# Kernel tuning notes

Measured on AMD Instinct MI355X. Metric: run time of the kernel, lower is better.

The kernel has to match this reference:

```python
import jax, jax.numpy as jnp
import numpy as np

EPS_NORM = 1e-12  # F.normalize eps
SINK_EPS = 0.1    # entropic regularization
THRESH = 0.01
MAX_ITERS = 100


def _l2_normalize(x):
    n = jnp.linalg.norm(x, axis=1, keepdims=True)
    return x / jnp.maximum(n, EPS_NORM)


def _sinkhorn(K, u, v):
    # K: [M, N], u: [M], v: [N]. Mirrors the torch loop with early stop on err < thresh.
    def cond(state):
        i, r, c, err = state
        return jnp.logical_and(i < MAX_ITERS, err >= THRESH)

    def body(state):
        i, r, c, _ = state
        r0 = r
        r = u / (K @ c)          # [M]
        c = v / (K.T @ r)        # [N]
        err = jnp.mean(jnp.abs(r - r0))
        return (i + 1, r, c, err)

    init = (jnp.int32(0), jnp.ones_like(u), jnp.ones_like(v), jnp.float32(1e9))
    _, r, c, _ = jax.lax.while_loop(cond, body, init)
    return jnp.outer(r, c) * K   # [M, N]


def _ot(src, tgt):
    # src: [M, D] (gt cluster centers), tgt: [N, D] (local features)
    s = _l2_normalize(src)
    t = _l2_normalize(tgt)
    sim = s @ t.T                         # [M, N], differentiable
    M, N = sim.shape
    u = jnp.full((M,), 1.0 / M, sim.dtype)
    v = jnp.full((N,), 1.0 / N, sim.dtype)
    K = jax.lax.stop_gradient(jnp.exp(-(1.0 - sim) / SINK_EPS))  # no_grad in torch
    T = jax.lax.stop_gradient(_sinkhorn(K, u, v))
    return jnp.sum(T * sim)


def setup_inputs() -> dict:
    key = jax.random.key(0)
    k1, k2, k3, k4 = jax.random.split(key, 4)
    E, B, D = 3, 4096, 1024
    M, N = 5, 256
    return {
        "feature": jax.random.normal(k1, (E, B, D), jnp.float32),
        "gt": jax.random.normal(k2, (E, B, D), jnp.float32),
        "gt_local": jax.random.normal(k3, (E, M, D), jnp.float32),
        "feature_local": jax.random.normal(k4, (E, N, D), jnp.float32),
    }


def reference(feature, gt, gt_local, feature_local):
    E = feature.shape[0]
    # global term: (1/E) * sum_e mean_b sum_d feature*gt
    loss_global = jnp.mean(jnp.sum(feature * gt, axis=-1))
    # local OT term per extractor: OT(gt_local, feature_local) * 2, then / E
    ot_vals = jax.vmap(_ot)(gt_local, feature_local)  # [E]
    loss_local = jnp.sum(ot_vals * 2.0) / E
    return loss_global + loss_local * 0.1
```

## Files before the change

### kernel.cpp

```cpp
#include <hip/hip_runtime.h>
#include <math.h>

#define NSIM_BLOCKS 48
#define NDOT_BLOCKS 512
#define TOTAL_F4 3145728

__global__ __launch_bounds__(256) void fused_main(
    const float4* __restrict__ f4, const float4* __restrict__ g4,
    const float* __restrict__ gt_local, const float* __restrict__ feat_local,
    float* __restrict__ ws_partials, float* __restrict__ ws_sim)
{
    __shared__ float s_sh[5 * 1024];
    __shared__ float rns_sh[5];
    __shared__ float red_sh[4];
    const int tid = threadIdx.x;
    const int lane = tid & 63;
    const int wid = tid >> 6;

    if (blockIdx.x < NSIM_BLOCKS) {
        const int b = blockIdx.x;
        const int e = b >> 4;
        const int chunk = b & 15;
        const float* sbase = gt_local + e * 5 * 1024;
        for (int idx = tid; idx < 5120; idx += 256) s_sh[idx] = sbase[idx];
        __syncthreads();
        for (int m = wid; m < 5; m += 4) {
            float acc = 0.f;
            #pragma unroll
            for (int k = 0; k < 16; ++k) {
                float v = s_sh[m * 1024 + lane + 64 * k];
                acc += v * v;
            }
            #pragma unroll
            for (int o = 32; o; o >>= 1) acc += __shfl_xor(acc, o);
            if (lane == 0) rns_sh[m] = 1.f / fmaxf(sqrtf(acc), 1e-12f);
        }
        __syncthreads();
        for (int rr = 0; rr < 4; ++rr) {
            const int n = chunk * 16 + wid * 4 + rr;
            const float* trow = feat_local + (e * 256 + n) * 1024;
            float a0 = 0.f, a1 = 0.f, a2 = 0.f, a3 = 0.f, a4 = 0.f, at = 0.f;
            #pragma unroll
            for (int k = 0; k < 16; ++k) {
                const int d = lane + 64 * k;
                const float tv = trow[d];
                at += tv * tv;
                a0 += tv * s_sh[d];
                a1 += tv * s_sh[1024 + d];
                a2 += tv * s_sh[2048 + d];
                a3 += tv * s_sh[3072 + d];
                a4 += tv * s_sh[4096 + d];
            }
            #pragma unroll
            for (int o = 32; o; o >>= 1) {
                at += __shfl_xor(at, o);
                a0 += __shfl_xor(a0, o);
                a1 += __shfl_xor(a1, o);
                a2 += __shfl_xor(a2, o);
                a3 += __shfl_xor(a3, o);
                a4 += __shfl_xor(a4, o);
            }
            if (lane == 0) {
                const float rnt = 1.f / fmaxf(sqrtf(at), 1e-12f);
                float* dst = ws_sim + e * 5 * 256 + n;
                dst[0]    = a0 * rns_sh[0] * rnt;
                dst[256]  = a1 * rns_sh[1] * rnt;
                dst[512]  = a2 * rns_sh[2] * rnt;
                dst[768]  = a3 * rns_sh[3] * rnt;
                dst[1024] = a4 * rns_sh[4] * rnt;
            }
        }
    } else {
        const int d = blockIdx.x - NSIM_BLOCKS;
        float acc = 0.f;
        const int stride = NDOT_BLOCKS * 256;
        for (int i = d * 256 + tid; i < TOTAL_F4; i += stride) {
            const float4 a = f4[i];
            const float4 b = g4[i];
            acc += a.x * b.x + a.y * b.y + a.z * b.z + a.w * b.w;
        }
        #pragma unroll
        for (int o = 32; o; o >>= 1) acc += __shfl_xor(acc, o);
        if (lane == 0) red_sh[wid] = acc;
        __syncthreads();
        if (tid == 0)
            ws_partials[d] = red_sh[0] + red_sh[1] + red_sh[2] + red_sh[3];
    }
}

__global__ __launch_bounds__(256) void finalize_kernel(
    const float* __restrict__ ws_partials, const float* __restrict__ ws_sim,
    float* __restrict__ out)
{
    __shared__ float ot_sh[3];
    __shared__ double g_sh;
    const int tid = threadIdx.x;
    const int lane = tid & 63;
    const int wid = tid >> 6;

    if (wid < 3) {
        const int e = wid;
        float K[5][4], S[5][4];
        #pragma unroll
        for (int m = 0; m < 5; ++m)
            #pragma unroll
            for (int j = 0; j < 4; ++j) {
                const float s = ws_sim[(e * 5 + m) * 256 + lane + 64 * j];
                S[m][j] = s;
                K[m][j] = expf(-(1.0f - s) / 0.1f);
            }
        float r[5] = {1.f, 1.f, 1.f, 1.f, 1.f};
        float c[4] = {1.f, 1.f, 1.f, 1.f};
        float err;
        int it = 0;
        do {
            float r0[5];
            #pragma unroll
            for (int m = 0; m < 5; ++m) r0[m] = r[m];
            #pragma unroll
            for (int m = 0; m < 5; ++m) {
                float p = K[m][0] * c[0] + K[m][1] * c[1] +
                          K[m][2] * c[2] + K[m][3] * c[3];
                #pragma unroll
                for (int o = 32; o; o >>= 1) p += __shfl_xor(p, o);
                r[m] = 0.2f / p;
            }
            #pragma unroll
            for (int j = 0; j < 4; ++j) {
                const float q = K[0][j] * r[0] + K[1][j] * r[1] +
                                K[2][j] * r[2] + K[3][j] * r[3] +
                                K[4][j] * r[4];
                c[j] = (1.0f / 256.0f) / q;
            }
            err = (fabsf(r[0] - r0[0]) + fabsf(r[1] - r0[1]) +
                   fabsf(r[2] - r0[2]) + fabsf(r[3] - r0[3]) +
                   fabsf(r[4] - r0[4])) * 0.2f;
            ++it;
        } while (it < 100 && err >= 0.01f);

        float ot = 0.f;
        #pragma unroll
        for (int m = 0; m < 5; ++m)
            #pragma unroll
            for (int j = 0; j < 4; ++j)
                ot += r[m] * c[j] * K[m][j] * S[m][j];
        #pragma unroll
        for (int o = 32; o; o >>= 1) ot += __shfl_xor(ot, o);
        if (lane == 0) ot_sh[e] = ot;
    } else {
        double acc = 0.0;
        #pragma unroll
        for (int k = 0; k < 8; ++k) acc += (double)ws_partials[lane + 64 * k];
        #pragma unroll
        for (int o = 32; o; o >>= 1) acc += __shfl_xor(acc, o);
        if (lane == 0) g_sh = acc;
    }
    __syncthreads();
    if (tid == 0) {
        const float loss_global = (float)(g_sh / 12288.0);
        const float loss_local = (ot_sh[0] + ot_sh[1] + ot_sh[2]) * 2.0f / 3.0f;
        out[0] = loss_global + 0.1f * loss_local;
    }
}

extern "C" void kernel_launch(void* const* d_in, const int* in_sizes, int n_in,
                              void* d_out, int out_size, void* d_ws, size_t ws_size,
                              hipStream_t stream) {
    const float4* f4 = (const float4*)d_in[0];
    const float4* g4 = (const float4*)d_in[1];
    const float* gt_local = (const float*)d_in[2];
    const float* feat_local = (const float*)d_in[3];
    float* ws_partials = (float*)d_ws;
    float* ws_sim = ws_partials + NDOT_BLOCKS;
    float* out = (float*)d_out;

    hipLaunchKernelGGL(fused_main, dim3(NSIM_BLOCKS + NDOT_BLOCKS), dim3(256), 0,
                       stream, f4, g4, gt_local, feat_local, ws_partials, ws_sim);
    hipLaunchKernelGGL(finalize_kernel, dim3(1), dim3(256), 0, stream,
                       ws_partials, ws_sim, out);
}
```

Baseline: 124.4 us.

## Fully unroll global dot with nontemporal loads across more blocks, prenormalize src rows

The global dot-product part now uses 2048 blocks, and each thread issues six independent nontemporal float4 load pairs up front instead of running a strided loop. The aim is more memory-level parallelism and less cache pollution on the 100 MB streaming read. The sim blocks now load the cluster centers as vectors and normalize them in shared memory once, which removes the per-output rescaling. The finalize kernel reads four times as many partials, and the code depends on the fixed total size being exactly 6 × 2048 × 256 float4 elements.

```diff
diff --git a/kernel.cpp b/kernel.cpp
--- a/kernel.cpp
+++ b/kernel.cpp
@@ -1,28 +1,57 @@
 #include <hip/hip_runtime.h>
 #include <math.h>
 
+typedef float f32x4 __attribute__((ext_vector_type(4)));
+
 #define NSIM_BLOCKS 48
-#define NDOT_BLOCKS 512
+#define NDOT_BLOCKS 2048
+#define THREADS 256
 #define TOTAL_F4 3145728
+#define DOT_STRIDE (NDOT_BLOCKS * THREADS)
 
 __global__ __launch_bounds__(256) void fused_main(
-    const float4* __restrict__ f4, const float4* __restrict__ g4,
+    const f32x4* __restrict__ f4, const f32x4* __restrict__ g4,
     const float* __restrict__ gt_local, const float* __restrict__ feat_local,
     float* __restrict__ ws_partials, float* __restrict__ ws_sim)
 {
-    __shared__ float s_sh[5 * 1024];
-    __shared__ float rns_sh[5];
-    __shared__ float red_sh[4];
+    __shared__ float s_sh[5120];
     const int tid = threadIdx.x;
     const int lane = tid & 63;
     const int wid = tid >> 6;
 
-    if (blockIdx.x < NSIM_BLOCKS) {
-        const int b = blockIdx.x;
-        const int e = b >> 4;
-        const int chunk = b & 15;
-        const float* sbase = gt_local + e * 5 * 1024;
-        for (int idx = tid; idx < 5120; idx += 256) s_sh[idx] = sbase[idx];
+    if (blockIdx.x >= NSIM_BLOCKS) {
+        const int base = (blockIdx.x - NSIM_BLOCKS) * THREADS + tid;
+        f32x4 a0 = __builtin_nontemporal_load(&f4[base + 0 * DOT_STRIDE]);
+        f32x4 b0 = __builtin_nontemporal_load(&g4[base + 0 * DOT_STRIDE]);
+        f32x4 a1 = __builtin_nontemporal_load(&f4[base + 1 * DOT_STRIDE]);
+        f32x4 b1 = __builtin_nontemporal_load(&g4[base + 1 * DOT_STRIDE]);
+        f32x4 a2 = __builtin_nontemporal_load(&f4[base + 2 * DOT_STRIDE]);
+        f32x4 b2 = __builtin_nontemporal_load(&g4[base + 2 * DOT_STRIDE]);
+        f32x4 a3 = __builtin_nontemporal_load(&f4[base + 3 * DOT_STRIDE]);
+        f32x4 b3 = __builtin_nontemporal_load(&g4[base + 3 * DOT_STRIDE]);
+        f32x4 a4 = __builtin_nontemporal_load(&f4[base + 4 * DOT_STRIDE]);
+        f32x4 b4 = __builtin_nontemporal_load(&g4[base + 4 * DOT_STRIDE]);
+        f32x4 a5 = __builtin_nontemporal_load(&f4[base + 5 * DOT_STRIDE]);
+        f32x4 b5 = __builtin_nontemporal_load(&g4[base + 5 * DOT_STRIDE]);
+        f32x4 p0 = a0 * b0 + a1 * b1;
+        f32x4 p1 = a2 * b2 + a3 * b3;
+        f32x4 p2 = a4 * b4 + a5 * b5;
+        f32x4 p = p0 + p1 + p2;
+        float acc = p.x + p.y + p.z + p.w;
+        #pragma unroll
+        for (int o = 32; o; o >>= 1) acc += __shfl_xor(acc, o);
+        if (lane == 0) s_sh[wid] = acc;
+        __syncthreads();
+        if (tid == 0)
+            ws_partials[blockIdx.x - NSIM_BLOCKS] =
+                s_sh[0] + s_sh[1] + s_sh[2] + s_sh[3];
+    } else {
+        const int e = blockIdx.x >> 4;
+        const int chunk = blockIdx.x & 15;
+        const f32x4* sbase = (const f32x4*)(gt_local + e * 5120);
+        #pragma unroll
+        for (int k = 0; k < 5; ++k)
+            ((f32x4*)s_sh)[tid + 256 * k] = sbase[tid + 256 * k];
         __syncthreads();
         for (int m = wid; m < 5; m += 4) {
             float acc = 0.f;
@@ -33,7 +62,10 @@
             }
             #pragma unroll
             for (int o = 32; o; o >>= 1) acc += __shfl_xor(acc, o);
-            if (lane == 0) rns_sh[m] = 1.f / fmaxf(sqrtf(acc), 1e-12f);
+            const float rinv = 1.f / fmaxf(sqrtf(acc), 1e-12f);
+            #pragma unroll
+            for (int k = 0; k < 16; ++k)
+                s_sh[m * 1024 + lane + 64 * k] *= rinv;
         }
         __syncthreads();
         for (int rr = 0; rr < 4; ++rr) {
@@ -63,28 +95,13 @@
             if (lane == 0) {
                 const float rnt = 1.f / fmaxf(sqrtf(at), 1e-12f);
                 float* dst = ws_sim + e * 5 * 256 + n;
-                dst[0]    = a0 * rns_sh[0] * rnt;
-                dst[256]  = a1 * rns_sh[1] * rnt;
-                dst[512]  = a2 * rns_sh[2] * rnt;
-                dst[768]  = a3 * rns_sh[3] * rnt;
-                dst[1024] = a4 * rns_sh[4] * rnt;
+                dst[0]    = a0 * rnt;
+                dst[256]  = a1 * rnt;
+                dst[512]  = a2 * rnt;
+                dst[768]  = a3 * rnt;
+                dst[1024] = a4 * rnt;
             }
         }
-    } else {
-        const int d = blockIdx.x - NSIM_BLOCKS;
-        float acc = 0.f;
-        const int stride = NDOT_BLOCKS * 256;
-        for (int i = d * 256 + tid; i < TOTAL_F4; i += stride) {
-            const float4 a = f4[i];
-            const float4 b = g4[i];
-            acc += a.x * b.x + a.y * b.y + a.z * b.z + a.w * b.w;
-        }
-        #pragma unroll
-        for (int o = 32; o; o >>= 1) acc += __shfl_xor(acc, o);
-        if (lane == 0) red_sh[wid] = acc;
-        __syncthreads();
-        if (tid == 0)
-            ws_partials[d] = red_sh[0] + red_sh[1] + red_sh[2] + red_sh[3];
     }
 }
 
@@ -150,7 +167,7 @@
     } else {
         double acc = 0.0;
         #pragma unroll
-        for (int k = 0; k < 8; ++k) acc += (double)ws_partials[lane + 64 * k];
+        for (int k = 0; k < 32; ++k) acc += (double)ws_partials[lane + 64 * k];
         #pragma unroll
         for (int o = 32; o; o >>= 1) acc += __shfl_xor(acc, o);
         if (lane == 0) g_sh = acc;
@@ -166,16 +183,16 @@
 extern "C" void kernel_launch(void* const* d_in, const int* in_sizes, int n_in,
                               void* d_out, int out_size, void* d_ws, size_t ws_size,
                               hipStream_t stream) {
-    const float4* f4 = (const float4*)d_in[0];
-    const float4* g4 = (const float4*)d_in[1];
+    const f32x4* f4 = (const f32x4*)d_in[0];
+    const f32x4* g4 = (const f32x4*)d_in[1];
     const float* gt_local = (const float*)d_in[2];
     const float* feat_local = (const float*)d_in[3];
     float* ws_partials = (float*)d_ws;
     float* ws_sim = ws_partials + NDOT_BLOCKS;
     float* out = (float*)d_out;
 
-    hipLaunchKernelGGL(fused_main, dim3(NSIM_BLOCKS + NDOT_BLOCKS), dim3(256), 0,
-                       stream, f4, g4, gt_local, feat_local, ws_partials, ws_sim);
-    hipLaunchKernelGGL(finalize_kernel, dim3(1), dim3(256), 0, stream,
+    hipLaunchKernelGGL(fused_main, dim3(NSIM_BLOCKS + NDOT_BLOCKS), dim3(THREADS),
+                       0, stream, f4, g4, gt_local, feat_local, ws_partials, ws_sim);
+    hipLaunchKernelGGL(finalize_kernel, dim3(1), dim3(THREADS), 0, stream,
                        ws_partials, ws_sim, out);
 }
```

New measurement: 131.6 us. 5.8% more time.
